# Kernel optimization log

Measured on AMD Instinct MI355X. Metric: run time of the kernel, lower is better.

The kernel has to match this reference:

```python
import jax, jax.numpy as jnp
import numpy as np

NUM_BITS = 4
BLOCK = 64
IN_F = 4096
OUT_F = 4096
RANK = 16


def dequantize(packed_qweight, weight_max, lookup_table):
    """Unpack sub-byte indices from uint8 bytes, lookup codebook, apply per-block absmax scale.
    packed_qweight: [n_bytes, 1] uint8; weight_max: [n_blocks]; lookup_table: [2**NUM_BITS].
    Returns dequantized weight [OUT_F, IN_F]."""
    nipb = 8 // NUM_BITS  # indices per byte
    mask = (1 << NUM_BITS) - 1
    b = packed_qweight[:, 0]
    # index i was packed at bit position i*NUM_BITS (LSB first)
    idx = jnp.stack([(b >> (i * NUM_BITS)) & mask for i in range(nipb)], axis=-1).reshape(-1)
    w = lookup_table[idx].reshape(-1, BLOCK) * weight_max[:, None]  # [n_blocks, BLOCK]
    return w.reshape(OUT_F, IN_F)


def setup_inputs() -> dict:
    key = jax.random.key(0)
    k0, k1, k2, k3, k4, k5 = jax.random.split(key, 6)
    x = jax.random.normal(k0, (4, 2048, IN_F), dtype=jnp.float32)
    packed_qweight = jax.random.randint(k1, (OUT_F * IN_F // (8 // NUM_BITS), 1), 0, 256, dtype=jnp.int32).astype(jnp.uint8)
    weight_max = jax.random.uniform(k2, (OUT_F * IN_F // BLOCK,), dtype=jnp.float32, minval=0.01, maxval=0.1)
    # uniform non-symmetric codebook: linspace(-1, 1, 2**num_bits)
    lookup_table = jnp.linspace(-1.0, 1.0, 2 ** NUM_BITS, dtype=jnp.float32)
    lora_A = jax.random.normal(k3, (RANK, IN_F), dtype=jnp.float32) * 0.02
    lora_B = jax.random.normal(k4, (OUT_F, RANK), dtype=jnp.float32) * 0.02
    bias = jax.random.normal(k5, (OUT_F,), dtype=jnp.float32) * 0.02
    return {"x": x, "packed_qweight": packed_qweight, "weight_max": weight_max,
            "lookup_table": lookup_table, "lora_A": lora_A, "lora_B": lora_B, "bias": bias}


def reference(x, packed_qweight, weight_max, lookup_table, lora_A, lora_B, bias):
    W = dequantize(packed_qweight, weight_max, lookup_table)  # [OUT_F, IN_F]
    base = jnp.einsum('bsi,oi->bso', x, W)
    lora = jnp.einsum('bsr,or->bso', jnp.einsum('bsi,ri->bsr', x, lora_A), lora_B)
    return base + lora + bias
```

## Files before the change

kernel.cpp:

```cpp
#include <hip/hip_runtime.h>
#include <hip/hip_bf16.h>
#include <stdint.h>

constexpr int IN_F  = 4096;
constexpr int OUT_F = 4096;
constexpr int M_ROWS = 4 * 2048;
constexpr int RANK = 16;

typedef short short8 __attribute__((ext_vector_type(8)));
typedef float f32x4 __attribute__((ext_vector_type(4)));

__device__ __forceinline__ short f2bf(float f) {
  return __builtin_bit_cast(short, __float2bfloat16(f));
}

__device__ __forceinline__ void gload16(const void* g, void* l) {
  __builtin_amdgcn_global_load_lds(
      (const __attribute__((address_space(1))) void*)g,
      (__attribute__((address_space(3))) void*)l, 16, 0, 0);
}

__global__ __launch_bounds__(256) void dequant_lora_kernel(
    const int* __restrict__ q,
    const float* __restrict__ wmax,
    const float* __restrict__ lut,
    const float* __restrict__ lA,
    const float* __restrict__ lB,
    __hip_bfloat16* __restrict__ W) {
  __shared__ float slut[16];
  if (threadIdx.x < 16) slut[threadIdx.x] = lut[threadIdx.x];
  __syncthreads();

  const int o0  = blockIdx.y * 64 + (threadIdx.x >> 5) * 8;
  const int ib0 = blockIdx.x * 512 + (threadIdx.x & 31) * 16;

  #pragma unroll
  for (int h = 0; h < 2; ++h) {
    const int ib = ib0 + h * 8;
    float w[8][8];
    #pragma unroll
    for (int p = 0; p < 8; ++p) {
      const size_t l = (size_t)(o0 + p) * IN_F + ib;
      const int4 u = *(const int4*)(q + (l >> 1));
      const float sc = wmax[l >> 6];
      w[p][0] = slut[u.x & 15] * sc;
      w[p][1] = slut[(u.x >> 4) & 15] * sc;
      w[p][2] = slut[u.y & 15] * sc;
      w[p][3] = slut[(u.y >> 4) & 15] * sc;
      w[p][4] = slut[u.z & 15] * sc;
      w[p][5] = slut[(u.z >> 4) & 15] * sc;
      w[p][6] = slut[u.w & 15] * sc;
      w[p][7] = slut[(u.w >> 4) & 15] * sc;
    }
    #pragma unroll 2
    for (int r = 0; r < 16; ++r) {
      const float* ar = lA + (size_t)r * IN_F + ib;
      const float4 a0 = *(const float4*)(ar);
      const float4 a1 = *(const float4*)(ar + 4);
      float b[8];
      #pragma unroll
      for (int p = 0; p < 8; ++p) b[p] = lB[(size_t)(o0 + p) * RANK + r];
      #pragma unroll
      for (int p = 0; p < 8; ++p) {
        w[p][0] += b[p] * a0.x; w[p][1] += b[p] * a0.y;
        w[p][2] += b[p] * a0.z; w[p][3] += b[p] * a0.w;
        w[p][4] += b[p] * a1.x; w[p][5] += b[p] * a1.y;
        w[p][6] += b[p] * a1.z; w[p][7] += b[p] * a1.w;
      }
    }
    #pragma unroll
    for (int p = 0; p < 8; ++p) {
      short8 s;
      #pragma unroll
      for (int qq = 0; qq < 8; ++qq) s[qq] = f2bf(w[p][qq]);
      *(short8*)&W[(size_t)(o0 + p) * IN_F + ib] = s;
    }
  }
}

__global__ __launch_bounds__(256) void cvt_x_kernel(
    const float* __restrict__ x, __hip_bfloat16* __restrict__ xb) {
  constexpr int NG = (M_ROWS * IN_F) / 8;
  const int stride = gridDim.x * blockDim.x;
  for (int i = blockIdx.x * blockDim.x + threadIdx.x; i < NG; i += stride) {
    const float4 a = ((const float4*)x)[2 * i];
    const float4 b = ((const float4*)x)[2 * i + 1];
    short8 s;
    s[0] = f2bf(a.x); s[1] = f2bf(a.y); s[2] = f2bf(a.z); s[3] = f2bf(a.w);
    s[4] = f2bf(b.x); s[5] = f2bf(b.y); s[6] = f2bf(b.z); s[7] = f2bf(b.w);
    ((short8*)xb)[i] = s;
  }
}

constexpr int BM = 256, BN = 256, BK = 64;
constexpr int GM = M_ROWS, GN = OUT_F, GK = IN_F;
constexpr int NKT = GK / BK;

#define LOAD_B(BUF, KH)                                                   \
  _Pragma("unroll")                                                       \
  for (int n_ = 0; n_ < 4; ++n_)                                          \
    bf[n_] = *(const short8*)&sB[BUF][KH][wn * 64 + n_ * 16 + lr][swr * 8];

#define LOAD_A(BUF, KH, MH)                                               \
  _Pragma("unroll")                                                       \
  for (int i_ = 0; i_ < 4; ++i_)                                          \
    af[i_] = *(const short8*)&sA[BUF][KH][wm * 128 + (MH) * 64 + i_ * 16 + lr][swr * 8];

#define MFMA_Q(MH)                                                        \
  __builtin_amdgcn_s_setprio(1);                                          \
  _Pragma("unroll")                                                       \
  for (int i_ = 0; i_ < 4; ++i_)                                          \
    _Pragma("unroll")                                                     \
    for (int n_ = 0; n_ < 4; ++n_)                                        \
      acc[(MH) * 4 + i_][n_] = __builtin_amdgcn_mfma_f32_16x16x32_bf16(   \
          af[i_], bf[n_], acc[(MH) * 4 + i_][n_], 0, 0, 0);               \
  __builtin_amdgcn_s_setprio(0);

#define PHASE(BUF, KH, MH, DOB, GB, LB, VM)                               \
  do {                                                                    \
    if (DOB) { LOAD_B(BUF, KH) }                                          \
    LOAD_A(BUF, KH, MH)                                                   \
    stage(GB, LB);                                                        \
    if (VM) asm volatile("s_waitcnt vmcnt(6)" ::: "memory");              \
    __builtin_amdgcn_s_barrier();                                         \
    MFMA_Q(MH)                                                            \
    __builtin_amdgcn_sched_barrier(0);                                    \
    __builtin_amdgcn_s_barrier();                                         \
  } while (0)

__global__ __launch_bounds__(512, 2) void gemm_bt_8phase(
    const __hip_bfloat16* __restrict__ A,
    const __hip_bfloat16* __restrict__ B,
    const float* __restrict__ bias,
    float* __restrict__ C) {
  __shared__ __hip_bfloat16 sA[2][2][256][32];
  __shared__ __hip_bfloat16 sB[2][2][256][32];

  const int tid  = threadIdx.x;
  const int lane = tid & 63;
  const int wave = tid >> 6;
  const int lr = lane & 15;
  const int lk = lane >> 4;
  const int wm = wave >> 2;
  const int wn = wave & 3;
  const int swr = lk ^ ((lr >> 1) & 3);

  const int bid = blockIdx.x;
  const int cpx = gridDim.x >> 3;
  const int wg  = (bid & 7) * cpx + (bid >> 3);
  const int nbn = GN / BN;
  const int m0 = (wg / nbn) * BM;
  const int n0 = (wg % nbn) * BN;

  const __hip_bfloat16* Abase = A + (size_t)m0 * GK;
  const __hip_bfloat16* Bbase = B + (size_t)n0 * GK;

  const int swst = (tid >> 3) & 3;
  auto stage = [&](const __hip_bfloat16* gb, __hip_bfloat16* lb) {
    #pragma unroll
    for (int j = 0; j < 2; ++j) {
      const int c = j * 512 + tid;
      const int row = c >> 2, slot = c & 3;
      const int sg = slot ^ swst;
      gload16(gb + (size_t)row * GK + sg * 8,
              (void*)((char*)lb + (j * 512 + wave * 64) * 16));
    }
  };

  f32x4 acc[8][4];
  #pragma unroll
  for (int m = 0; m < 8; ++m)
    #pragma unroll
    for (int n = 0; n < 4; ++n) acc[m][n] = (f32x4)0.0f;

  stage(Abase +  0, &sA[0][0][0][0]);
  stage(Bbase +  0, &sB[0][0][0][0]);
  stage(Abase + 32, &sA[0][1][0][0]);
  stage(Bbase + 32, &sB[0][1][0][0]);
  stage(Bbase + 64, &sB[1][0][0][0]);
  stage(Abase + 64, &sA[1][0][0][0]);
  stage(Bbase + 96, &sB[1][1][0][0]);
  asm volatile("s_waitcnt vmcnt(6)" ::: "memory");
  __builtin_amdgcn_s_barrier();

  short8 af[4], bf[4];

  for (int t = 0; t < NKT; t += 2) {
    const int t2 = (t + 2 < NKT) ? t + 2 : NKT - 1;
    const int t3 = (t + 3 < NKT) ? t + 3 : NKT - 1;

    PHASE(0, 0, 0, true,  Abase + (size_t)(t + 1) * 64 + 32, &sA[1][1][0][0], false);
    PHASE(0, 0, 1, false, Bbase + (size_t)t2 * 64,           &sB[0][0][0][0], false);
    PHASE(0, 1, 0, true,  Abase + (size_t)t2 * 64,           &sA[0][0][0][0], false);
    PHASE(0, 1, 1, false, Bbase + (size_t)t2 * 64 + 32,      &sB[0][1][0][0], true);
    PHASE(1, 0, 0, true,  Abase + (size_t)t2 * 64 + 32,      &sA[0][1][0][0], false);
    PHASE(1, 0, 1, false, Bbase + (size_t)t3 * 64,           &sB[1][0][0][0], false);
    PHASE(1, 1, 0, true,  Abase + (size_t)t3 * 64,           &sA[1][0][0][0], false);
    PHASE(1, 1, 1, false, Bbase + (size_t)t3 * 64 + 32,      &sB[1][1][0][0], true);
  }

  #pragma unroll
  for (int n = 0; n < 4; ++n) {
    const int col = n0 + wn * 64 + n * 16 + lr;
    const float bv = bias[col];
    #pragma unroll
    for (int m = 0; m < 8; ++m) {
      const int row = m0 + wm * 128 + m * 16 + lk * 4;
      #pragma unroll
      for (int j = 0; j < 4; ++j)
        C[(size_t)(row + j) * GN + col] = acc[m][n][j] + bv;
    }
  }
}

extern "C" void kernel_launch(void* const* d_in, const int* in_sizes, int n_in,
                              void* d_out, int out_size, void* d_ws, size_t ws_size,
                              hipStream_t stream) {
  const float* x    = (const float*)d_in[0];
  const int*   qw   = (const int*)d_in[1];
  const float* wmax = (const float*)d_in[2];
  const float* lut  = (const float*)d_in[3];
  const float* lA   = (const float*)d_in[4];
  const float* lB   = (const float*)d_in[5];
  const float* bias = (const float*)d_in[6];
  float* out = (float*)d_out;

  __hip_bfloat16* Weff = (__hip_bfloat16*)d_ws;
  __hip_bfloat16* xb   = (__hip_bfloat16*)((char*)d_ws + (size_t)OUT_F * IN_F * 2);

  dequant_lora_kernel<<<dim3(IN_F / 512, OUT_F / 64), 256, 0, stream>>>(
      qw, wmax, lut, lA, lB, Weff);
  cvt_x_kernel<<<2048, 256, 0, stream>>>(x, xb);
  gemm_bt_8phase<<<(GM / BM) * (GN / BN), 512, 0, stream>>>(xb, Weff, bias, out);
}
```

Before: 328.2 us.

## Replace 8-phase double-buffered GEMM with 4-stage ring-buffered K pipeline

Restructures the bf16 GEMM main loop from an 8-phase schedule over two double-buffered K=64 tiles into a 4-slot ring of K=32 tiles, staying 3 tiles ahead. Each tile step uses one wait and one barrier, issues loads for tile t+3, then reads all 8 A fragments and 4 B fragments and runs 32 MFMAs. This drops half of the per-phase barriers and the split A/B fragment reuse. In exchange it holds more fragment registers live and loses the finer interleaving of LDS reads with MFMAs.

```diff
diff --git a/kernel.cpp b/kernel.cpp
--- a/kernel.cpp
+++ b/kernel.cpp
@@ -92,49 +92,42 @@
   }
 }
 
-constexpr int BM = 256, BN = 256, BK = 64;
+constexpr int BM = 256, BN = 256, BK = 32;
 constexpr int GM = M_ROWS, GN = OUT_F, GK = IN_F;
 constexpr int NKT = GK / BK;
 
-#define LOAD_B(BUF, KH)                                                   \
-  _Pragma("unroll")                                                       \
-  for (int n_ = 0; n_ < 4; ++n_)                                          \
-    bf[n_] = *(const short8*)&sB[BUF][KH][wn * 64 + n_ * 16 + lr][swr * 8];
-
-#define LOAD_A(BUF, KH, MH)                                               \
-  _Pragma("unroll")                                                       \
-  for (int i_ = 0; i_ < 4; ++i_)                                          \
-    af[i_] = *(const short8*)&sA[BUF][KH][wm * 128 + (MH) * 64 + i_ * 16 + lr][swr * 8];
-
-#define MFMA_Q(MH)                                                        \
-  __builtin_amdgcn_s_setprio(1);                                          \
-  _Pragma("unroll")                                                       \
-  for (int i_ = 0; i_ < 4; ++i_)                                          \
-    _Pragma("unroll")                                                     \
-    for (int n_ = 0; n_ < 4; ++n_)                                        \
-      acc[(MH) * 4 + i_][n_] = __builtin_amdgcn_mfma_f32_16x16x32_bf16(   \
-          af[i_], bf[n_], acc[(MH) * 4 + i_][n_], 0, 0, 0);               \
-  __builtin_amdgcn_s_setprio(0);
-
-#define PHASE(BUF, KH, MH, DOB, GB, LB, VM)                               \
-  do {                                                                    \
-    if (DOB) { LOAD_B(BUF, KH) }                                          \
-    LOAD_A(BUF, KH, MH)                                                   \
-    stage(GB, LB);                                                        \
-    if (VM) asm volatile("s_waitcnt vmcnt(6)" ::: "memory");              \
-    __builtin_amdgcn_s_barrier();                                         \
-    MFMA_Q(MH)                                                            \
-    __builtin_amdgcn_sched_barrier(0);                                    \
-    __builtin_amdgcn_s_barrier();                                         \
+#define TILE(BUF, T)                                                       \
+  do {                                                                     \
+    asm volatile("s_waitcnt vmcnt(8)" ::: "memory");                       \
+    __builtin_amdgcn_s_barrier();                                          \
+    __builtin_amdgcn_sched_barrier(0);                                     \
+    const int ts_ = ((T) + 3 < NKT) ? (T) + 3 : NKT - 1;                   \
+    stage(Abase + (size_t)ts_ * BK, &sA[((BUF) + 3) & 3][0][0]);           \
+    stage(Bbase + (size_t)ts_ * BK, &sB[((BUF) + 3) & 3][0][0]);           \
+    short8 af[8], bf[4];                                                   \
+    _Pragma("unroll")                                                      \
+    for (int n_ = 0; n_ < 4; ++n_)                                         \
+      bf[n_] = *(const short8*)&sB[BUF][wn * 64 + n_ * 16 + lr][swr * 8];  \
+    _Pragma("unroll")                                                      \
+    for (int m_ = 0; m_ < 8; ++m_)                                         \
+      af[m_] = *(const short8*)&sA[BUF][wm * 128 + m_ * 16 + lr][swr * 8]; \
+    __builtin_amdgcn_s_setprio(1);                                         \
+    _Pragma("unroll")                                                      \
+    for (int m_ = 0; m_ < 8; ++m_)                                         \
+      _Pragma("unroll")                                                    \
+      for (int n_ = 0; n_ < 4; ++n_)                                       \
+        acc[m_][n_] = __builtin_amdgcn_mfma_f32_16x16x32_bf16(             \
+            af[m_], bf[n_], acc[m_][n_], 0, 0, 0);                         \
+    __builtin_amdgcn_s_setprio(0);                                         \
   } while (0)
 
-__global__ __launch_bounds__(512, 2) void gemm_bt_8phase(
+__global__ __launch_bounds__(512, 2) void gemm_bt_ring(
     const __hip_bfloat16* __restrict__ A,
     const __hip_bfloat16* __restrict__ B,
     const float* __restrict__ bias,
     float* __restrict__ C) {
-  __shared__ __hip_bfloat16 sA[2][2][256][32];
-  __shared__ __hip_bfloat16 sB[2][2][256][32];
+  __shared__ __hip_bfloat16 sA[4][256][32];
+  __shared__ __hip_bfloat16 sB[4][256][32];
 
   const int tid  = threadIdx.x;
   const int lane = tid & 63;
@@ -173,30 +166,18 @@
     #pragma unroll
     for (int n = 0; n < 4; ++n) acc[m][n] = (f32x4)0.0f;
 
-  stage(Abase +  0, &sA[0][0][0][0]);
-  stage(Bbase +  0, &sB[0][0][0][0]);
-  stage(Abase + 32, &sA[0][1][0][0]);
-  stage(Bbase + 32, &sB[0][1][0][0]);
-  stage(Bbase + 64, &sB[1][0][0][0]);
-  stage(Abase + 64, &sA[1][0][0][0]);
-  stage(Bbase + 96, &sB[1][1][0][0]);
-  asm volatile("s_waitcnt vmcnt(6)" ::: "memory");
-  __builtin_amdgcn_s_barrier();
-
-  short8 af[4], bf[4];
-
-  for (int t = 0; t < NKT; t += 2) {
-    const int t2 = (t + 2 < NKT) ? t + 2 : NKT - 1;
-    const int t3 = (t + 3 < NKT) ? t + 3 : NKT - 1;
-
-    PHASE(0, 0, 0, true,  Abase + (size_t)(t + 1) * 64 + 32, &sA[1][1][0][0], false);
-    PHASE(0, 0, 1, false, Bbase + (size_t)t2 * 64,           &sB[0][0][0][0], false);
-    PHASE(0, 1, 0, true,  Abase + (size_t)t2 * 64,           &sA[0][0][0][0], false);
-    PHASE(0, 1, 1, false, Bbase + (size_t)t2 * 64 + 32,      &sB[0][1][0][0], true);
-    PHASE(1, 0, 0, true,  Abase + (size_t)t2 * 64 + 32,      &sA[0][1][0][0], false);
-    PHASE(1, 0, 1, false, Bbase + (size_t)t3 * 64,           &sB[1][0][0][0], false);
-    PHASE(1, 1, 0, true,  Abase + (size_t)t3 * 64,           &sA[1][0][0][0], false);
-    PHASE(1, 1, 1, false, Bbase + (size_t)t3 * 64 + 32,      &sB[1][1][0][0], true);
+  stage(Abase +  0, &sA[0][0][0]);
+  stage(Bbase +  0, &sB[0][0][0]);
+  stage(Abase + 32, &sA[1][0][0]);
+  stage(Bbase + 32, &sB[1][0][0]);
+  stage(Abase + 64, &sA[2][0][0]);
+  stage(Bbase + 64, &sB[2][0][0]);
+
+  for (int t = 0; t < NKT; t += 4) {
+    TILE(0, t);
+    TILE(1, t + 1);
+    TILE(2, t + 2);
+    TILE(3, t + 3);
   }
 
   #pragma unroll
@@ -231,5 +212,5 @@
   dequant_lora_kernel<<<dim3(IN_F / 512, OUT_F / 64), 256, 0, stream>>>(
       qw, wmax, lut, lA, lB, Weff);
   cvt_x_kernel<<<2048, 256, 0, stream>>>(x, xb);
-  gemm_bt_8phase<<<(GM / BM) * (GN / BN), 512, 0, stream>>>(xb, Weff, bias, out);
-}
+  gemm_bt_ring<<<(GM / BM) * (GN / BN), 512, 0, stream>>>(xb, Weff, bias, out);
+}
```

Result: slower. 339.6 us (+3.5%).

## Merge prep kernels into one launch and use single barrier per GEMM phase

Applied to the files above, without the earlier changes.

Fuses the dequant+LoRA kernel and the x-to-bf16 conversion into one launch by splitting the grid by block index, which removes one kernel launch and lets the two independent prep jobs run concurrently. The GEMM phase is reordered to wait and barrier first, then issue the next global->LDS stage, LDS reads and MFMAs, dropping the trailing barrier so each phase has one barrier instead of two. The risk is a write-after-read hazard on LDS if the stage into a buffer can overlap reads of the same buffer from slower waves. The prologue barrier was also removed.

```diff
diff --git a/kernel.cpp b/kernel.cpp
--- a/kernel.cpp
+++ b/kernel.cpp
@@ -20,75 +20,78 @@
       (__attribute__((address_space(3))) void*)l, 16, 0, 0);
 }
 
-__global__ __launch_bounds__(256) void dequant_lora_kernel(
+__global__ __launch_bounds__(256) void prep_kernel(
     const int* __restrict__ q,
     const float* __restrict__ wmax,
     const float* __restrict__ lut,
     const float* __restrict__ lA,
     const float* __restrict__ lB,
-    __hip_bfloat16* __restrict__ W) {
-  __shared__ float slut[16];
-  if (threadIdx.x < 16) slut[threadIdx.x] = lut[threadIdx.x];
-  __syncthreads();
-
-  const int o0  = blockIdx.y * 64 + (threadIdx.x >> 5) * 8;
-  const int ib0 = blockIdx.x * 512 + (threadIdx.x & 31) * 16;
-
-  #pragma unroll
-  for (int h = 0; h < 2; ++h) {
-    const int ib = ib0 + h * 8;
-    float w[8][8];
-    #pragma unroll
-    for (int p = 0; p < 8; ++p) {
-      const size_t l = (size_t)(o0 + p) * IN_F + ib;
-      const int4 u = *(const int4*)(q + (l >> 1));
-      const float sc = wmax[l >> 6];
-      w[p][0] = slut[u.x & 15] * sc;
-      w[p][1] = slut[(u.x >> 4) & 15] * sc;
-      w[p][2] = slut[u.y & 15] * sc;
-      w[p][3] = slut[(u.y >> 4) & 15] * sc;
-      w[p][4] = slut[u.z & 15] * sc;
-      w[p][5] = slut[(u.z >> 4) & 15] * sc;
-      w[p][6] = slut[u.w & 15] * sc;
-      w[p][7] = slut[(u.w >> 4) & 15] * sc;
-    }
-    #pragma unroll 2
-    for (int r = 0; r < 16; ++r) {
-      const float* ar = lA + (size_t)r * IN_F + ib;
-      const float4 a0 = *(const float4*)(ar);
-      const float4 a1 = *(const float4*)(ar + 4);
-      float b[8];
-      #pragma unroll
-      for (int p = 0; p < 8; ++p) b[p] = lB[(size_t)(o0 + p) * RANK + r];
+    const float* __restrict__ x,
+    __hip_bfloat16* __restrict__ W,
+    __hip_bfloat16* __restrict__ xb) {
+  if (blockIdx.x < 512) {
+    __shared__ float slut[16];
+    if (threadIdx.x < 16) slut[threadIdx.x] = lut[threadIdx.x];
+    __syncthreads();
+
+    const int bx = blockIdx.x & 7, by = blockIdx.x >> 3;
+    const int o0  = by * 64 + (threadIdx.x >> 5) * 8;
+    const int ib0 = bx * 512 + (threadIdx.x & 31) * 16;
+
+    #pragma unroll
+    for (int h = 0; h < 2; ++h) {
+      const int ib = ib0 + h * 8;
+      float w[8][8];
       #pragma unroll
       for (int p = 0; p < 8; ++p) {
-        w[p][0] += b[p] * a0.x; w[p][1] += b[p] * a0.y;
-        w[p][2] += b[p] * a0.z; w[p][3] += b[p] * a0.w;
-        w[p][4] += b[p] * a1.x; w[p][5] += b[p] * a1.y;
-        w[p][6] += b[p] * a1.z; w[p][7] += b[p] * a1.w;
+        const size_t l = (size_t)(o0 + p) * IN_F + ib;
+        const int4 u = *(const int4*)(q + (l >> 1));
+        const float sc = wmax[l >> 6];
+        w[p][0] = slut[u.x & 15] * sc;
+        w[p][1] = slut[(u.x >> 4) & 15] * sc;
+        w[p][2] = slut[u.y & 15] * sc;
+        w[p][3] = slut[(u.y >> 4) & 15] * sc;
+        w[p][4] = slut[u.z & 15] * sc;
+        w[p][5] = slut[(u.z >> 4) & 15] * sc;
+        w[p][6] = slut[u.w & 15] * sc;
+        w[p][7] = slut[(u.w >> 4) & 15] * sc;
       }
-    }
-    #pragma unroll
-    for (int p = 0; p < 8; ++p) {
+      #pragma unroll 2
+      for (int r = 0; r < 16; ++r) {
+        const float* ar = lA + (size_t)r * IN_F + ib;
+        const float4 a0 = *(const float4*)(ar);
+        const float4 a1 = *(const float4*)(ar + 4);
+        float b[8];
+        #pragma unroll
+        for (int p = 0; p < 8; ++p) b[p] = lB[(size_t)(o0 + p) * RANK + r];
+        #pragma unroll
+        for (int p = 0; p < 8; ++p) {
+          w[p][0] += b[p] * a0.x; w[p][1] += b[p] * a0.y;
+          w[p][2] += b[p] * a0.z; w[p][3] += b[p] * a0.w;
+          w[p][4] += b[p] * a1.x; w[p][5] += b[p] * a1.y;
+          w[p][6] += b[p] * a1.z; w[p][7] += b[p] * a1.w;
+        }
+      }
+      #pragma unroll
+      for (int p = 0; p < 8; ++p) {
+        short8 s;
+        #pragma unroll
+        for (int qq = 0; qq < 8; ++qq) s[qq] = f2bf(w[p][qq]);
+        *(short8*)&W[(size_t)(o0 + p) * IN_F + ib] = s;
+      }
+    }
+  } else {
+    constexpr int NG = (M_ROWS * IN_F) / 8;
+    const int nblk = 2048;
+    const int stride = nblk * 256;
+    for (int i = (blockIdx.x - 512) * 256 + threadIdx.x; i < NG; i += stride) {
+      const float4 a = ((const float4*)x)[2 * i];
+      const float4 b = ((const float4*)x)[2 * i + 1];
       short8 s;
-      #pragma unroll
-      for (int qq = 0; qq < 8; ++qq) s[qq] = f2bf(w[p][qq]);
-      *(short8*)&W[(size_t)(o0 + p) * IN_F + ib] = s;
-    }
-  }
-}
-
-__global__ __launch_bounds__(256) void cvt_x_kernel(
-    const float* __restrict__ x, __hip_bfloat16* __restrict__ xb) {
-  constexpr int NG = (M_ROWS * IN_F) / 8;
-  const int stride = gridDim.x * blockDim.x;
-  for (int i = blockIdx.x * blockDim.x + threadIdx.x; i < NG; i += stride) {
-    const float4 a = ((const float4*)x)[2 * i];
-    const float4 b = ((const float4*)x)[2 * i + 1];
-    short8 s;
-    s[0] = f2bf(a.x); s[1] = f2bf(a.y); s[2] = f2bf(a.z); s[3] = f2bf(a.w);
-    s[4] = f2bf(b.x); s[5] = f2bf(b.y); s[6] = f2bf(b.z); s[7] = f2bf(b.w);
-    ((short8*)xb)[i] = s;
+      s[0] = f2bf(a.x); s[1] = f2bf(a.y); s[2] = f2bf(a.z); s[3] = f2bf(a.w);
+      s[4] = f2bf(b.x); s[5] = f2bf(b.y); s[6] = f2bf(b.z); s[7] = f2bf(b.w);
+      ((short8*)xb)[i] = s;
+    }
   }
 }
 
@@ -118,17 +121,16 @@
 
 #define PHASE(BUF, KH, MH, DOB, GB, LB, VM)                               \
   do {                                                                    \
+    if (VM) asm volatile("s_waitcnt vmcnt(6)" ::: "memory");              \
+    __builtin_amdgcn_s_barrier();                                         \
+    stage(GB, LB);                                                        \
     if (DOB) { LOAD_B(BUF, KH) }                                          \
     LOAD_A(BUF, KH, MH)                                                   \
-    stage(GB, LB);                                                        \
-    if (VM) asm volatile("s_waitcnt vmcnt(6)" ::: "memory");              \
-    __builtin_amdgcn_s_barrier();                                         \
     MFMA_Q(MH)                                                            \
     __builtin_amdgcn_sched_barrier(0);                                    \
-    __builtin_amdgcn_s_barrier();                                         \
   } while (0)
 
-__global__ __launch_bounds__(512, 2) void gemm_bt_8phase(
+__global__ __launch_bounds__(512, 2) void gemm_bt_1bar(
     const __hip_bfloat16* __restrict__ A,
     const __hip_bfloat16* __restrict__ B,
     const float* __restrict__ bias,
@@ -181,7 +183,6 @@
   stage(Abase + 64, &sA[1][0][0][0]);
   stage(Bbase + 96, &sB[1][1][0][0]);
   asm volatile("s_waitcnt vmcnt(6)" ::: "memory");
-  __builtin_amdgcn_s_barrier();
 
   short8 af[4], bf[4];
 
@@ -228,8 +229,6 @@
   __hip_bfloat16* Weff = (__hip_bfloat16*)d_ws;
   __hip_bfloat16* xb   = (__hip_bfloat16*)((char*)d_ws + (size_t)OUT_F * IN_F * 2);
 
-  dequant_lora_kernel<<<dim3(IN_F / 512, OUT_F / 64), 256, 0, stream>>>(
-      qw, wmax, lut, lA, lB, Weff);
-  cvt_x_kernel<<<2048, 256, 0, stream>>>(x, xb);
-  gemm_bt_8phase<<<(GM / BM) * (GN / BN), 512, 0, stream>>>(xb, Weff, bias, out);
-}
+  prep_kernel<<<2560, 256, 0, stream>>>(qw, wmax, lut, lA, lB, x, Weff, xb);
+  gemm_bt_1bar<<<(GM / BM) * (GN / BN), 512, 0, stream>>>(xb, Weff, bias, out);
+}
```

New measurement: 323.4 us. Within noise of the previous version (-1.4%).
